# Performance work log

Hardware: AMD Instinct MI355X
Metric: run time of the kernel (lower is better)

The kernel has to match this reference:

```python
import jax, jax.numpy as jnp
import numpy as np

N_HEADS, N_KV_HEADS, HEAD_DIM = 32, 8, 128
N_REP = N_HEADS // N_KV_HEADS


def apply_rope(x, cos, sin):
    # x: [B, H, T, D]; cos/sin: [T, D/2]. Interleaved complex rotation (LLaMA style).
    x1 = x[..., 0::2]
    x2 = x[..., 1::2]
    c = cos[None, None, :, :]
    s = sin[None, None, :, :]
    r1 = x1 * c - x2 * s
    r2 = x1 * s + x2 * c
    return jnp.stack([r1, r2], axis=-1).reshape(x.shape)


def setup_inputs() -> dict:
    key = jax.random.key(0)
    ks = jax.random.split(key, 7)
    B, T, D = 1, 2048, 4096
    sc = 0.02
    return {
        "x": jax.random.normal(ks[0], (B, T, D), jnp.float32),
        "cos": jnp.cos(jax.random.normal(ks[1], (T, HEAD_DIM // 2), jnp.float32)),
        "sin": jnp.sin(jax.random.normal(ks[1], (T, HEAD_DIM // 2), jnp.float32)),
        "wq": jax.random.normal(ks[2], (D, D), jnp.float32) * sc,
        "wk": jax.random.normal(ks[3], (N_KV_HEADS * HEAD_DIM, D), jnp.float32) * sc,
        "wv": jax.random.normal(ks[4], (N_KV_HEADS * HEAD_DIM, D), jnp.float32) * sc,
        "wo": jax.random.normal(ks[5], (D, D), jnp.float32) * sc,
    }


def reference(x, cos, sin, wq, wk, wv, wo):
    B, T, _ = x.shape
    # QKV projections (nn.Linear: y = x @ W^T)
    q = (x @ wq.T).reshape(B, T, N_HEADS, HEAD_DIM).transpose(0, 2, 1, 3)
    k = (x @ wk.T).reshape(B, T, N_KV_HEADS, HEAD_DIM).transpose(0, 2, 1, 3)
    v = (x @ wv.T).reshape(B, T, N_KV_HEADS, HEAD_DIM).transpose(0, 2, 1, 3)
    # RoPE on q, k
    q = apply_rope(q, cos[:T], sin[:T])
    k = apply_rope(k, cos[:T], sin[:T])
    # GQA: repeat_interleave kv heads along head dim
    if N_REP > 1:
        k = jnp.repeat(k, N_REP, axis=1)
        v = jnp.repeat(v, N_REP, axis=1)
    # causal SDPA
    scale = 1.0 / jnp.sqrt(jnp.float32(HEAD_DIM))
    scores = jnp.einsum("bhqd,bhkd->bhqk", q, k) * scale
    causal = jnp.tril(jnp.ones((T, T), dtype=bool))
    scores = jnp.where(causal[None, None], scores, jnp.finfo(scores.dtype).min)
    attn = jax.nn.softmax(scores, axis=-1)
    y = jnp.einsum("bhqk,bhkd->bhqd", attn, v)
    y = y.transpose(0, 2, 1, 3).reshape(B, T, -1)
    return y @ wo.T
```

## Files before the change

### kernel.cpp

```cpp
#include <hip/hip_runtime.h>
#include <stdint.h>

typedef unsigned short ushort_t;
typedef __attribute__((ext_vector_type(8))) __bf16 bf16x8;
typedef __attribute__((ext_vector_type(4))) float f32x4;
typedef __attribute__((ext_vector_type(16))) float f32x16;

#define MFMA16(a, b, c) __builtin_amdgcn_mfma_f32_16x16x32_bf16((a), (b), (c), 0, 0, 0)
#define MFMA32(a, b, c) __builtin_amdgcn_mfma_f32_32x32x16_bf16((a), (b), (c), 0, 0, 0)

#define STR_(x) #x
#define STR(x) STR_(x)

__device__ __forceinline__ ushort_t f2bf(float f) {
    unsigned u = __float_as_uint(f);
    u += 0x7fffu + ((u >> 16) & 1u);
    return (ushort_t)(u >> 16);
}

typedef __attribute__((address_space(1))) const unsigned char g_u8;
typedef __attribute__((address_space(3))) unsigned char l_u8;
__device__ __forceinline__ void gload16(const void* g, void* l) {
    __builtin_amdgcn_global_load_lds((g_u8*)g, (l_u8*)(unsigned int)(uintptr_t)l, 16, 0, 0);
}

__global__ __launch_bounds__(256) void cast_multi(const float* __restrict__ x,
                                                  const float* __restrict__ wq,
                                                  const float* __restrict__ wk,
                                                  const float* __restrict__ wv,
                                                  ushort_t* __restrict__ xb,
                                                  ushort_t* __restrict__ wqb,
                                                  ushort_t* __restrict__ wkb,
                                                  ushort_t* __restrict__ wvb) {
    int i = blockIdx.x * 256 + threadIdx.x;
    const float* in; ushort_t* out; int off;
    if (i < 2097152)      { in = x;  out = xb;  off = i; }
    else if (i < 6291456) { in = wq; out = wqb; off = i - 2097152; }
    else if (i < 7340032) { in = wk; out = wkb; off = i - 6291456; }
    else                  { in = wv; out = wvb; off = i - 7340032; }
    float4 v = ((const float4*)in)[off];
    ushort4 o;
    o.x = f2bf(v.x); o.y = f2bf(v.y); o.z = f2bf(v.z); o.w = f2bf(v.w);
    ((ushort4*)out)[off] = o;
}

__global__ __launch_bounds__(256) void cast_f32_bf16(const float* __restrict__ in,
                                                     ushort_t* __restrict__ out, int n4) {
    int i = blockIdx.x * 256 + threadIdx.x;
    if (i < n4) {
        float4 v = ((const float4*)in)[i];
        ushort4 o;
        o.x = f2bf(v.x); o.y = f2bf(v.y); o.z = f2bf(v.z); o.w = f2bf(v.w);
        ((ushort4*)out)[i] = o;
    }
}

#define GEMM_K_LOOP_8P(Aarr, Barr, KDIM, AI, BJ, ALOADS, BLOADS, VM)                     \
    const int l32 = lane & 31, hi = lane >> 5, r7 = l32 & 7;                             \
    const int srow = tid >> 3;                                                           \
    const int skc = (tid & 7) ^ (srow & 7);                                              \
    const ushort_t* aS = (Aarr) + (size_t)(bm + srow) * (KDIM) + skc * 8;                \
    const ushort_t* bS = (Barr) + (size_t)(bn + srow) * (KDIM) + skc * 8;                \
    const int lofs = tid * 8;                                                            \
    const int NT = (KDIM) >> 6;                                                          \
    _Pragma("unroll")                                                                    \
    for (int p = 0; p < (ALOADS); p++)                                                   \
        gload16(aS + (size_t)p * 64 * (KDIM), &Asl[0][lofs + p * 4096]);                 \
    _Pragma("unroll")                                                                    \
    for (int p = 0; p < (BLOADS); p++)                                                   \
        gload16(bS + (size_t)p * 64 * (KDIM), &Bsl[0][lofs + p * 4096]);                 \
    _Pragma("unroll")                                                                    \
    for (int p = 0; p < (BLOADS); p++)                                                   \
        gload16(bS + (size_t)p * 64 * (KDIM) + 64, &Bsl[1][lofs + p * 4096]);            \
    asm volatile("s_waitcnt vmcnt(" STR(VM) ")" ::: "memory");                           \
    __builtin_amdgcn_s_barrier();                                                        \
    asm volatile("" ::: "memory");                                                       \
    int cbB = 0, sbB = 2;                                                                \
    for (int t = 0; t < NT; t++) {                                                       \
        const int cbA = t & 1;                                                           \
        const ushort_t* Ab = Asl[cbA];                                                   \
        const ushort_t* Bb = Bsl[cbB];                                                   \
        ushort_t* AbS = Asl[cbA ^ 1];                                                    \
        ushort_t* BbS = Bsl[sbB];                                                        \
        const bool stA = (t + 1 < NT);                                                   \
        const bool stB = (t + 2 < NT);                                                   \
        const size_t koA = (size_t)(t + 1) * 64;                                         \
        const size_t koB = (size_t)(t + 2) * 64;                                         \
        _Pragma("unroll")                                                                \
        for (int ks = 0; ks < 4; ks++) {                                                 \
            const int swz = ((ks * 2 + hi) ^ r7) << 3;                                   \
            bf16x8 af[AI], bfr[BJ];                                                      \
            _Pragma("unroll")                                                            \
            for (int i = 0; i < (AI); i++)                                               \
                af[i] = *(const bf16x8*)(&Ab[(wm + i * 32 + l32) * 64 + swz]);           \
            _Pragma("unroll")                                                            \
            for (int j = 0; j < (BJ); j++)                                               \
                bfr[j] = *(const bf16x8*)(&Bb[(wn + j * 32 + l32) * 64 + swz]);          \
            if (ks == 0 && stA) {                                                        \
                _Pragma("unroll")                                                        \
                for (int p = 0; p < (ALOADS) / 2; p++)                                   \
                    gload16(aS + koA + (size_t)p * 64 * (KDIM), &AbS[lofs + p * 4096]);  \
            }                                                                            \
            if (ks == 1 && stA) {                                                        \
                _Pragma("unroll")                                                        \
                for (int p = (ALOADS) / 2; p < (ALOADS); p++)                            \
                    gload16(aS + koA + (size_t)p * 64 * (KDIM), &AbS[lofs + p * 4096]);  \
            }                                                                            \
            if (ks == 2 && stB) {                                                        \
                _Pragma("unroll")                                                        \
                for (int p = 0; p < (BLOADS) / 2; p++)                                   \
                    gload16(bS + koB + (size_t)p * 64 * (KDIM), &BbS[lofs + p * 4096]);  \
            }                                                                            \
            if (ks == 3 && stB) {                                                        \
                _Pragma("unroll")                                                        \
                for (int p = (BLOADS) / 2; p < (BLOADS); p++)                            \
                    gload16(bS + koB + (size_t)p * 64 * (KDIM), &BbS[lofs + p * 4096]);  \
            }                                                                            \
            __builtin_amdgcn_s_barrier();                                                \
            asm volatile("s_waitcnt lgkmcnt(0)" ::: "memory");                           \
            __builtin_amdgcn_sched_barrier(0);                                           \
            __builtin_amdgcn_s_setprio(1);                                               \
            _Pragma("unroll")                                                            \
            for (int i = 0; i < (AI); i++) {                                             \
                _Pragma("unroll")                                                        \
                for (int j = 0; j < (BJ); j++)                                           \
                    acc[i][j] = MFMA32(af[i], bfr[j], acc[i][j]);                        \
            }                                                                            \
            __builtin_amdgcn_s_setprio(0);                                               \
            if (ks < 3) {                                                                \
                __builtin_amdgcn_s_barrier();                                            \
            } else {                                                                     \
                if (stB) { asm volatile("s_waitcnt vmcnt(" STR(VM) ")" ::: "memory"); }  \
                else     { asm volatile("s_waitcnt vmcnt(0)" ::: "memory"); }            \
                __builtin_amdgcn_s_barrier();                                            \
                asm volatile("" ::: "memory");                                           \
                __builtin_amdgcn_sched_barrier(0);                                       \
            }                                                                            \
        }                                                                                \
        if (++cbB == 3) cbB = 0;                                                         \
        if (++sbB == 3) sbB = 0;                                                         \
    }

__global__ __launch_bounds__(512, 2) void gemm_qkv(const ushort_t* __restrict__ A,
                                                   const ushort_t* __restrict__ Wq,
                                                   const ushort_t* __restrict__ Wk,
                                                   const ushort_t* __restrict__ Wv,
                                                   ushort_t* __restrict__ Qo,
                                                   ushort_t* __restrict__ Ko,
                                                   ushort_t* __restrict__ VtO,
                                                   const float* __restrict__ cosp,
                                                   const float* __restrict__ sinp,
                                                   const float* __restrict__ wo,
                                                   ushort_t* __restrict__ wob) {
    const int by = blockIdx.y;
    const int tid = threadIdx.x;

    if (by >= 24) {
        const int ci = (by - 24) * gridDim.x + blockIdx.x;
        const float4* src = (const float4*)wo;
        ushort4* dst = (ushort4*)wob;
        int base = ci * 8192 + tid;
#pragma unroll
        for (int p = 0; p < 16; p++) {
            float4 v = src[base + p * 512];
            ushort4 o;
            o.x = f2bf(v.x); o.y = f2bf(v.y); o.z = f2bf(v.z); o.w = f2bf(v.w);
            dst[base + p * 512] = o;
        }
        return;
    }

    const ushort_t* B;
    int region, bn;
    if (by < 16)      { region = 0; B = Wq; bn = by * 256; }
    else if (by < 20) { region = 1; B = Wk; bn = (by - 16) * 256; }
    else              { region = 2; B = Wv; bn = (by - 20) * 256; }
    const int bm = blockIdx.x * 256;

    __shared__ __align__(16) ushort_t Asl[2][256 * 64];
    __shared__ __align__(16) ushort_t Bsl[3][256 * 64];
    const int w = tid >> 6, lane = tid & 63;
    const int wm = (w >> 2) * 128, wn = (w & 3) * 64;
    f32x16 acc[4][2] = {};

    GEMM_K_LOOP_8P(A, B, 4096, 4, 2, 4, 4, 4)

    const float qscale = 0.08838834764831845f;
    if (region < 2) {
        ushort_t* C = (region == 0) ? Qo : Ko;
        const int Nc = (region == 0) ? 4096 : 1024;
        const float scl = (region == 0) ? qscale : 1.0f;
#pragma unroll
        for (int i = 0; i < 4; i++)
#pragma unroll
            for (int j = 0; j < 2; j++) {
                const int col = bn + wn + j * 32 + l32;
                const int pj = (col & 127) >> 1;
#pragma unroll
                for (int r = 0; r < 16; r++) {
                    const int row = bm + wm + i * 32 + (r & 3) + 8 * (r >> 2) + 4 * hi;
                    float v = acc[i][j][r];
                    float p = __shfl_xor(v, 1);
                    float c = cosp[row * 64 + pj], s = sinp[row * 64 + pj];
                    float res = (col & 1) ? fmaf(p, s, v * c)
                                          : (v * c - p * s);
                    C[(size_t)row * Nc + col] = f2bf(res * scl);
                }
            }
    } else {
#pragma unroll
        for (int i = 0; i < 4; i++)
#pragma unroll
            for (int j = 0; j < 2; j++) {
                const int col = bn + wn + j * 32 + l32;
#pragma unroll
                for (int g = 0; g < 4; g++) {
                    const int rowb = bm + wm + i * 32 + g * 8 + 4 * hi;
                    ushort4 pk;
                    pk.x = f2bf(acc[i][j][g * 4 + 0]);
                    pk.y = f2bf(acc[i][j][g * 4 + 1]);
                    pk.z = f2bf(acc[i][j][g * 4 + 2]);
                    pk.w = f2bf(acc[i][j][g * 4 + 3]);
                    *(ushort4*)(VtO + (size_t)col * 2048 + rowb) = pk;
                }
            }
    }
}

__global__ __launch_bounds__(512, 2) void gemm_bt(const ushort_t* __restrict__ A,
                                                  const ushort_t* __restrict__ B,
                                                  float* __restrict__ C,
                                                  int M, int N, int K) {
    const int bm = blockIdx.x * 256, bn = blockIdx.y * 128;
    __shared__ __align__(16) ushort_t Asl[2][256 * 64];
    __shared__ __align__(16) ushort_t Bsl[3][128 * 64];
    const int tid = threadIdx.x;
    const int w = tid >> 6, lane = tid & 63;
    const int wm = (w >> 1) * 64, wn = (w & 1) * 64;
    f32x16 acc[2][2] = {};

    GEMM_K_LOOP_8P(A, B, K, 2, 2, 4, 2, 2)

#pragma unroll
    for (int i = 0; i < 2; i++)
#pragma unroll
        for (int j = 0; j < 2; j++) {
            const int col = bn + wn + j * 32 + l32;
#pragma unroll
            for (int r = 0; r < 16; r++) {
                const int row = bm + wm + i * 32 + (r & 3) + 8 * (r >> 2) + 4 * hi;
                C[(size_t)row * N + col] = acc[i][j][r];
            }
        }
}

__global__ __launch_bounds__(256) void flash_attn(const ushort_t* __restrict__ Q,
                                                  const ushort_t* __restrict__ Kp,
                                                  const ushort_t* __restrict__ Vt,
                                                  ushort_t* __restrict__ Y) {
    const int h = blockIdx.y, kh = h >> 2;
    const int tid = threadIdx.x;
    const int w = tid >> 6, lane = tid & 63;
    const int quad = lane >> 4, l16 = lane & 15;

    __shared__ __align__(16) ushort_t Ks[64 * 136];
    __shared__ __align__(16) ushort_t VtS[128 * 88];
    __shared__ __align__(16) ushort_t Ps[4 * 16 * 88];

    bf16x8 ones;
#pragma unroll
    for (int e = 0; e < 8; e++) ((ushort_t*)&ones)[e] = 0x3F80;

#pragma unroll 1
    for (int phase = 0; phase < 2; phase++) {
        const int qt = (phase == 0) ? blockIdx.x : 31 - blockIdx.x;

        bf16x8 qf[4];
        {
            const ushort_t* qrow = Q + (size_t)(qt * 64 + w * 16 + l16) * 4096 + h * 128 + quad * 8;
#pragma unroll
            for (int ks = 0; ks < 4; ks++) qf[ks] = *(const bf16x8*)(qrow + ks * 32);
        }

        f32x4 o[8] = {};
        f32x4 lacc = {};
        float m_i[4];
#pragma unroll
        for (int r = 0; r < 4; r++) m_i[r] = -1e30f;

        const int ntiles = qt + 1;
        for (int j = 0; j < ntiles; j++) {
            const int t0 = j * 64;
            {
#pragma unroll
                for (int p = 0; p < 4; p++) {
                    int ck = p * 256 + tid;
                    int r = ck >> 4, c = (ck & 15) * 8;
                    uint4 d = *(const uint4*)(Kp + (size_t)(t0 + r) * 1024 + kh * 128 + c);
                    *(uint4*)(&Ks[r * 136 + c]) = d;
                }
            }
            {
#pragma unroll
                for (int p = 0; p < 4; p++) {
                    int ck = p * 256 + tid;
                    int d = ck >> 3, c = (ck & 7) * 8;
                    uint4 v = *(const uint4*)(Vt + (size_t)(kh * 128 + d) * 2048 + t0 + c);
                    *(uint4*)(&VtS[d * 88 + c]) = v;
                }
            }
            __syncthreads();

            f32x4 s[4] = {};
#pragma unroll
            for (int ct = 0; ct < 4; ct++)
#pragma unroll
                for (int ks = 0; ks < 4; ks++) {
                    bf16x8 kf = *(const bf16x8*)(&Ks[(ct * 16 + l16) * 136 + ks * 32 + quad * 8]);
                    s[ct] = MFMA16(qf[ks], kf, s[ct]);
                }

            if (j == qt) {
#pragma unroll
                for (int ct = 0; ct < 4; ct++)
#pragma unroll
                    for (int r = 0; r < 4; r++) {
                        int rg = w * 16 + quad * 4 + r;
                        int cg = ct * 16 + l16;
                        if (cg > rg) s[ct][r] = -1e30f;
                    }
            }

            float alpha[4];
#pragma unroll
            for (int r = 0; r < 4; r++) {
                float v = fmaxf(fmaxf(s[0][r], s[1][r]), fmaxf(s[2][r], s[3][r]));
                v = fmaxf(v, __shfl_xor(v, 1));
                v = fmaxf(v, __shfl_xor(v, 2));
                v = fmaxf(v, __shfl_xor(v, 4));
                v = fmaxf(v, __shfl_xor(v, 8));
                float mn = fmaxf(m_i[r], v);
                alpha[r] = __expf(m_i[r] - mn);
                m_i[r] = mn;
            }
#pragma unroll
            for (int ct = 0; ct < 4; ct++)
#pragma unroll
                for (int r = 0; r < 4; r++)
                    s[ct][r] = __expf(s[ct][r] - m_i[r]);
#pragma unroll
            for (int n = 0; n < 8; n++)
#pragma unroll
                for (int r = 0; r < 4; r++) o[n][r] *= alpha[r];
#pragma unroll
            for (int r = 0; r < 4; r++) lacc[r] *= alpha[r];

#pragma unroll
            for (int ct = 0; ct < 4; ct++)
#pragma unroll
                for (int r = 0; r < 4; r++)
                    Ps[w * 1408 + (quad * 4 + r) * 88 + ct * 16 + l16] = f2bf(s[ct][r]);
            __threadfence_block();

#pragma unroll
            for (int ks2 = 0; ks2 < 2; ks2++) {
                bf16x8 pf = *(const bf16x8*)(&Ps[w * 1408 + l16 * 88 + ks2 * 32 + quad * 8]);
                lacc = MFMA16(pf, ones, lacc);
#pragma unroll
                for (int n = 0; n < 8; n++) {
                    bf16x8 vf = *(const bf16x8*)(&VtS[(n * 16 + l16) * 88 + ks2 * 32 + quad * 8]);
                    o[n] = MFMA16(pf, vf, o[n]);
                }
            }
            __syncthreads();
        }

        float inv[4];
#pragma unroll
        for (int r = 0; r < 4; r++) inv[r] = 1.0f / lacc[r];
#pragma unroll
        for (int n = 0; n < 8; n++)
#pragma unroll
            for (int r = 0; r < 4; r++) {
                int row = qt * 64 + w * 16 + quad * 4 + r;
                int col = h * 128 + n * 16 + l16;
                Y[(size_t)row * 4096 + col] = f2bf(o[n][r] * inv[r]);
            }
    }
}

extern "C" void kernel_launch(void* const* d_in, const int* in_sizes, int n_in,
                              void* d_out, int out_size, void* d_ws, size_t ws_size,
                              hipStream_t stream) {
    const float* x    = (const float*)d_in[0];
    const float* cosp = (const float*)d_in[1];
    const float* sinp = (const float*)d_in[2];
    const float* wq   = (const float*)d_in[3];
    const float* wk   = (const float*)d_in[4];
    const float* wv   = (const float*)d_in[5];
    const float* wo   = (const float*)d_in[6];
    float* out = (float*)d_out;

    ushort_t* xb   = (ushort_t*)d_ws;
    ushort_t* qb   = xb  + (size_t)2048 * 4096;
    ushort_t* yb   = qb  + (size_t)2048 * 4096;
    ushort_t* kb   = yb  + (size_t)2048 * 4096;
    ushort_t* vtb  = kb  + (size_t)2048 * 1024;
    ushort_t* wkb  = vtb + (size_t)1024 * 2048;
    ushort_t* wvb  = wkb + (size_t)1024 * 4096;
    ushort_t* wbig = wvb + (size_t)1024 * 4096;
    ushort_t* wob  = wbig + (size_t)4096 * 4096;
    const size_t need_fused = (size_t)(wob + (size_t)4096 * 4096 - xb) * sizeof(ushort_t);
    const bool fuse_wo = ws_size >= need_fused;

    cast_multi<<<32768, 256, 0, stream>>>(x, wq, wk, wv, xb, wbig, wkb, wvb);

    {
        dim3 g(8, fuse_wo ? 88 : 24, 1);
        gemm_qkv<<<g, 512, 0, stream>>>(xb, wbig, wkb, wvb, qb, kb, vtb, cosp, sinp,
                                        wo, fuse_wo ? wob : wbig);
    }

    {
        dim3 g(16, 32, 1);
        flash_attn<<<g, 256, 0, stream>>>(qb, kb, vtb, yb);
    }

    const ushort_t* wo_b = fuse_wo ? wob : wbig;
    if (!fuse_wo)
        cast_f32_bf16<<<16384, 256, 0, stream>>>(wo, wbig, 4096 * 4096 / 4);
    {
        dim3 g(8, 32, 1);
        gemm_bt<<<g, 512, 0, stream>>>(yb, wo_b, out, 2048, 4096, 4096);
    }
}
```

Before: 467.0 us.

## Use 128x128 single-buffered QKV GEMM tiles and prefetch K/V tiles in attention

```diff
diff --git a/kernel.cpp b/kernel.cpp
--- a/kernel.cpp
+++ b/kernel.cpp
@@ -54,6 +54,40 @@
         ((ushort4*)out)[i] = o;
     }
 }
+
+#define GEMM_K_LOOP(Aarr, Barr, KDIM)                                                   \
+    const ushort_t* aptr[4]; const ushort_t* bptr[4]; int ldsoff[4];                    \
+    _Pragma("unroll")                                                                   \
+    for (int p = 0; p < 4; p++) {                                                       \
+        int s = p * 256 + tid;                                                          \
+        int row = s >> 3;                                                               \
+        int kc = (s & 7) ^ (row & 7);                                                   \
+        aptr[p] = Aarr + (size_t)(bm + row) * (KDIM) + kc * 8;                          \
+        bptr[p] = Barr + (size_t)(bn + row) * (KDIM) + kc * 8;                          \
+        ldsoff[p] = s * 8;                                                              \
+    }                                                                                   \
+    const int l32 = lane & 31, hi = lane >> 5, r7 = l32 & 7;                            \
+    for (int k0 = 0; k0 < (KDIM); k0 += 64) {                                           \
+        _Pragma("unroll")                                                               \
+        for (int p = 0; p < 4; p++) {                                                   \
+            gload16(aptr[p] + k0, As + ldsoff[p]);                                      \
+            gload16(bptr[p] + k0, Bs + ldsoff[p]);                                      \
+        }                                                                               \
+        __syncthreads();                                                                \
+        _Pragma("unroll")                                                               \
+        for (int ks = 0; ks < 4; ks++) {                                                \
+            const int swz = ((ks * 2 + hi) ^ r7) << 3;                                  \
+            bf16x8 a0 = *(const bf16x8*)(&As[(wm + l32) * 64 + swz]);                   \
+            bf16x8 a1 = *(const bf16x8*)(&As[(wm + 32 + l32) * 64 + swz]);              \
+            bf16x8 b0 = *(const bf16x8*)(&Bs[(wn + l32) * 64 + swz]);                   \
+            bf16x8 b1 = *(const bf16x8*)(&Bs[(wn + 32 + l32) * 64 + swz]);              \
+            acc[0][0] = MFMA32(a0, b0, acc[0][0]);                                      \
+            acc[0][1] = MFMA32(a0, b1, acc[0][1]);                                      \
+            acc[1][0] = MFMA32(a1, b0, acc[1][0]);                                      \
+            acc[1][1] = MFMA32(a1, b1, acc[1][1]);                                      \
+        }                                                                               \
+        __syncthreads();                                                                \
+    }
 
 #define GEMM_K_LOOP_8P(Aarr, Barr, KDIM, AI, BJ, ALOADS, BLOADS, VM)                     \
     const int l32 = lane & 31, hi = lane >> 5, r7 = l32 & 7;                             \
@@ -141,7 +175,7 @@
         if (++sbB == 3) sbB = 0;                                                         \
     }
 
-__global__ __launch_bounds__(512, 2) void gemm_qkv(const ushort_t* __restrict__ A,
+__global__ __launch_bounds__(256, 3) void gemm_qkv(const ushort_t* __restrict__ A,
                                                    const ushort_t* __restrict__ Wq,
                                                    const ushort_t* __restrict__ Wk,
                                                    const ushort_t* __restrict__ Wv,
@@ -155,35 +189,35 @@
     const int by = blockIdx.y;
     const int tid = threadIdx.x;
 
-    if (by >= 24) {
-        const int ci = (by - 24) * gridDim.x + blockIdx.x;
+    if (by >= 48) {
+        const int ci = (by - 48) * gridDim.x + blockIdx.x;
         const float4* src = (const float4*)wo;
         ushort4* dst = (ushort4*)wob;
-        int base = ci * 8192 + tid;
+        int base = ci * 4096 + tid;
 #pragma unroll
         for (int p = 0; p < 16; p++) {
-            float4 v = src[base + p * 512];
+            float4 v = src[base + p * 256];
             ushort4 o;
             o.x = f2bf(v.x); o.y = f2bf(v.y); o.z = f2bf(v.z); o.w = f2bf(v.w);
-            dst[base + p * 512] = o;
+            dst[base + p * 256] = o;
         }
         return;
     }
 
     const ushort_t* B;
     int region, bn;
-    if (by < 16)      { region = 0; B = Wq; bn = by * 256; }
-    else if (by < 20) { region = 1; B = Wk; bn = (by - 16) * 256; }
-    else              { region = 2; B = Wv; bn = (by - 20) * 256; }
-    const int bm = blockIdx.x * 256;
-
-    __shared__ __align__(16) ushort_t Asl[2][256 * 64];
-    __shared__ __align__(16) ushort_t Bsl[3][256 * 64];
+    if (by < 32)      { region = 0; B = Wq; bn = by * 128; }
+    else if (by < 40) { region = 1; B = Wk; bn = (by - 32) * 128; }
+    else              { region = 2; B = Wv; bn = (by - 40) * 128; }
+    const int bm = blockIdx.x * 128;
+
+    __shared__ __align__(16) ushort_t As[128 * 64];
+    __shared__ __align__(16) ushort_t Bs[128 * 64];
     const int w = tid >> 6, lane = tid & 63;
-    const int wm = (w >> 2) * 128, wn = (w & 3) * 64;
-    f32x16 acc[4][2] = {};
-
-    GEMM_K_LOOP_8P(A, B, 4096, 4, 2, 4, 4, 4)
+    const int wm = (w >> 1) * 64, wn = (w & 1) * 64;
+    f32x16 acc[2][2] = {};
+
+    GEMM_K_LOOP(A, B, 4096)
 
     const float qscale = 0.08838834764831845f;
     if (region < 2) {
@@ -191,7 +225,7 @@
         const int Nc = (region == 0) ? 4096 : 1024;
         const float scl = (region == 0) ? qscale : 1.0f;
 #pragma unroll
-        for (int i = 0; i < 4; i++)
+        for (int i = 0; i < 2; i++)
 #pragma unroll
             for (int j = 0; j < 2; j++) {
                 const int col = bn + wn + j * 32 + l32;
@@ -209,7 +243,7 @@
             }
     } else {
 #pragma unroll
-        for (int i = 0; i < 4; i++)
+        for (int i = 0; i < 2; i++)
 #pragma unroll
             for (int j = 0; j < 2; j++) {
                 const int col = bn + wn + j * 32 + l32;
@@ -271,6 +305,24 @@
 #pragma unroll
     for (int e = 0; e < 8; e++) ((ushort_t*)&ones)[e] = 0x3F80;
 
+    uint4 kreg[4], vreg[4];
+    const int kr = tid >> 4, kc = (tid & 15) * 8;
+    const int vd = tid >> 3, vc = (tid & 7) * 8;
+    const ushort_t* kbase = Kp + (size_t)kr * 1024 + kh * 128 + kc;
+    const ushort_t* vbase = Vt + (size_t)(kh * 128 + vd) * 2048 + vc;
+
+#define LOAD_TILE(T0)                                                         \
+    {                                                                         \
+        _Pragma("unroll")                                                     \
+        for (int p = 0; p < 4; p++)                                           \
+            kreg[p] = *(const uint4*)(kbase + (size_t)((T0) + p * 16) * 1024);\
+        _Pragma("unroll")                                                     \
+        for (int p = 0; p < 4; p++)                                           \
+            vreg[p] = *(const uint4*)(vbase + (size_t)(p * 32) * 2048 + (T0));\
+    }
+
+    LOAD_TILE(0)
+
 #pragma unroll 1
     for (int phase = 0; phase < 2; phase++) {
         const int qt = (phase == 0) ? blockIdx.x : 31 - blockIdx.x;
@@ -290,26 +342,16 @@
 
         const int ntiles = qt + 1;
         for (int j = 0; j < ntiles; j++) {
-            const int t0 = j * 64;
-            {
-#pragma unroll
-                for (int p = 0; p < 4; p++) {
-                    int ck = p * 256 + tid;
-                    int r = ck >> 4, c = (ck & 15) * 8;
-                    uint4 d = *(const uint4*)(Kp + (size_t)(t0 + r) * 1024 + kh * 128 + c);
-                    *(uint4*)(&Ks[r * 136 + c]) = d;
-                }
-            }
-            {
-#pragma unroll
-                for (int p = 0; p < 4; p++) {
-                    int ck = p * 256 + tid;
-                    int d = ck >> 3, c = (ck & 7) * 8;
-                    uint4 v = *(const uint4*)(Vt + (size_t)(kh * 128 + d) * 2048 + t0 + c);
-                    *(uint4*)(&VtS[d * 88 + c]) = v;
-                }
-            }
+#pragma unroll
+            for (int p = 0; p < 4; p++)
+                *(uint4*)(&Ks[(kr + p * 16) * 136 + kc]) = kreg[p];
+#pragma unroll
+            for (int p = 0; p < 4; p++)
+                *(uint4*)(&VtS[(vd + p * 32) * 88 + vc]) = vreg[p];
             __syncthreads();
+
+            if (j + 1 < ntiles) { LOAD_TILE((j + 1) * 64) }
+            else if (phase == 0) { LOAD_TILE(0) }
 
             f32x4 s[4] = {};
 #pragma unroll
@@ -387,6 +429,7 @@
                 Y[(size_t)row * 4096 + col] = f2bf(o[n][r] * inv[r]);
             }
     }
+#undef LOAD_TILE
 }
 
 extern "C" void kernel_launch(void* const* d_in, const int* in_sizes, int n_in,
@@ -416,8 +459,8 @@
     cast_multi<<<32768, 256, 0, stream>>>(x, wq, wk, wv, xb, wbig, wkb, wvb);
 
     {
-        dim3 g(8, fuse_wo ? 88 : 24, 1);
-        gemm_qkv<<<g, 512, 0, stream>>>(xb, wbig, wkb, wvb, qb, kb, vtb, cosp, sinp,
+        dim3 g(16, fuse_wo ? 112 : 48, 1);
+        gemm_qkv<<<g, 256, 0, stream>>>(xb, wbig, wkb, wvb, qb, kb, vtb, cosp, sinp,
                                         wo, fuse_wo ? wob : wbig);
     }
 
```

Result: slower. 571.1 us (+22.3%).
